# Performance work log

Hardware: AMD Instinct MI355X
Metric: run time of the kernel (lower is better)

The kernel has to match this reference:

```python
import jax, jax.numpy as jnp
import numpy as np

N_NODES = 50000
N_EDGES = 800000
N_GRAPHS = 128
HIDDEN = 64
HEADS = 2
OUT = 4
NEG_SLOPE = 0.2
ALPHA_FLAG = 0.05


def _gat_conv(x, src, dst, W, a_src, a_dst, b):
    # PyG GATConv, concat=False (mean over heads), self-loops already appended.
    N = x.shape[0]
    H, C = a_src.shape
    xh = (x @ W).reshape(N, H, C)                       # [N,H,C]
    s_src = (xh * a_src).sum(-1)                        # [N,H]
    s_dst = (xh * a_dst).sum(-1)                        # [N,H]
    e = s_src[src] + s_dst[dst]                         # [E,H]
    e = jnp.where(e > 0, e, NEG_SLOPE * e)              # LeakyReLU(0.2)
    emax = jax.ops.segment_max(e, dst, num_segments=N)  # per-dst softmax max
    emax = jnp.where(jnp.isfinite(emax), emax, 0.0)
    p = jnp.exp(e - emax[dst])
    denom = jax.ops.segment_sum(p, dst, num_segments=N)
    alpha = p / (denom[dst] + 1e-16)                    # [E,H]
    out = jax.ops.segment_sum(alpha[:, :, None] * xh[src], dst, num_segments=N)
    return out.mean(axis=1) + b                         # [N,HIDDEN]


def setup_inputs() -> dict:
    key = jax.random.key(0)
    ks = jax.random.split(key, 32)
    f = lambda k, shape, s=0.1: (jax.random.normal(k, shape) * s).astype(jnp.float32)
    inp = {}
    inp['x_all'] = jax.random.normal(ks[0], (N_NODES, 8), dtype=jnp.float32)
    inp['climber'] = jax.random.normal(ks[1], (N_GRAPHS, 4), dtype=jnp.float32)
    inp['edge_index'] = jax.random.randint(ks[2], (2, N_EDGES), 0, N_NODES)
    inp['batch'] = jnp.sort(jax.random.randint(ks[3], (N_NODES,), 0, N_GRAPHS))
    H = HIDDEN
    inp['W_in'] = f(ks[4], (6, H)); inp['b_in'] = jnp.zeros((H,), jnp.float32)
    inp['W_c'] = f(ks[5], (4, H)); inp['b_c'] = jnp.zeros((H,), jnp.float32)
    inp['W_f1'] = f(ks[6], (H, 2 * H)); inp['b_f1'] = jnp.zeros((2 * H,), jnp.float32)
    inp['W_f2'] = f(ks[7], (H, 2 * H)); inp['b_f2'] = jnp.zeros((2 * H,), jnp.float32)
    inp['W_g1'] = f(ks[8], (H, HEADS * H)); inp['a_src1'] = f(ks[9], (HEADS, H)); inp['a_dst1'] = f(ks[10], (HEADS, H)); inp['b_g1'] = jnp.zeros((H,), jnp.float32)
    inp['W_g2'] = f(ks[11], (H, HEADS * H)); inp['a_src2'] = f(ks[12], (HEADS, H)); inp['a_dst2'] = f(ks[13], (HEADS, H)); inp['b_g2'] = jnp.zeros((H,), jnp.float32)
    inp['W_cl1'] = f(ks[14], (H, H)); inp['b_cl1'] = jnp.zeros((H,), jnp.float32)
    inp['W_cl2'] = f(ks[15], (H, OUT)); inp['b_cl2'] = jnp.zeros((OUT,), jnp.float32)
    inp['W_fh1'] = f(ks[16], (2, 8), 0.001); inp['b_fh1'] = jnp.zeros((8,), jnp.float32)
    inp['W_fh2'] = f(ks[17], (8, OUT), 0.001); inp['b_fh2'] = jnp.zeros((OUT,), jnp.float32)
    return inp


def reference(x_all, climber, edge_index, batch, W_in, b_in, W_c, b_c,
              W_f1, b_f1, W_f2, b_f2,
              W_g1, a_src1, a_dst1, b_g1,
              W_g2, a_src2, a_dst2, b_g2,
              W_cl1, b_cl1, W_cl2, b_cl2,
              W_fh1, b_fh1, W_fh2, b_fh2):
    N = x_all.shape[0]
    flags = x_all[:, -2:]
    x = x_all[:, :-2]
    # climber embedding (eval mode -> dropout is identity)
    c = jax.nn.relu(climber @ W_c + b_c)                 # [G,H]
    x = x @ W_in + b_in                                  # [N,H]
    # FiLM 1
    gb = c @ W_f1 + b_f1
    gamma, beta = jnp.split(gb, 2, axis=-1)
    x = x * (1.0 + gamma[batch]) + beta[batch]
    # add self-loops (PyG GATConv default)
    loop = jnp.arange(N, dtype=edge_index.dtype)
    src = jnp.concatenate([edge_index[0], loop])
    dst = jnp.concatenate([edge_index[1], loop])
    x = jax.nn.relu(_gat_conv(x, src, dst, W_g1, a_src1, a_dst1, b_g1))
    # FiLM 2
    gb = c @ W_f2 + b_f2
    gamma, beta = jnp.split(gb, 2, axis=-1)
    x = x * (1.0 + gamma[batch]) + beta[batch]
    x = jax.nn.relu(_gat_conv(x, src, dst, W_g2, a_src2, a_dst2, b_g2))
    logits_main = jax.nn.relu(x @ W_cl1 + b_cl1) @ W_cl2 + b_cl2
    logits_flag = jax.nn.relu(flags @ W_fh1 + b_fh1) @ W_fh2 + b_fh2
    return logits_main + ALPHA_FLAG * logits_flag
```

## Files before the change

### kernel.cpp

```cpp
#include <hip/hip_runtime.h>
#include <hip/hip_fp16.h>

#define NEG_SLOPE 0.2f
#define ALPHA_FLAG 0.05f

static inline size_t align256(size_t x) { return (x + 255) & ~(size_t)255; }

__global__ void prep_kernel(const float* __restrict__ climber,
                            const float* __restrict__ W_c, const float* __restrict__ b_c,
                            const float* __restrict__ W_f1, const float* __restrict__ b_f1,
                            const float* __restrict__ W_f2, const float* __restrict__ b_f2,
                            float* __restrict__ gb1, float* __restrict__ gb2) {
    __shared__ float c_sh[64];
    int g = blockIdx.x, t = threadIdx.x;
    if (t < 64) {
        float acc = b_c[t];
#pragma unroll
        for (int k = 0; k < 4; ++k) acc = fmaf(climber[g * 4 + k], W_c[k * 64 + t], acc);
        c_sh[t] = fmaxf(acc, 0.f);
    }
    __syncthreads();
    float a1 = b_f1[t], a2 = b_f2[t];
#pragma unroll 8
    for (int h = 0; h < 64; ++h) {
        float cv = c_sh[h];
        a1 = fmaf(cv, W_f1[h * 128 + t], a1);
        a2 = fmaf(cv, W_f2[h * 128 + t], a2);
    }
    gb1[g * 128 + t] = a1;
    gb2[g * 128 + t] = a2;
}

__global__ void node_in_kernel(const float* __restrict__ x_all, const int* __restrict__ batch,
                               const float* __restrict__ W_in, const float* __restrict__ b_in,
                               const float* __restrict__ gb1, float* __restrict__ x, int N) {
    int idx = blockIdx.x * blockDim.x + threadIdx.x;
    if (idx >= N * 64) return;
    int n = idx >> 6, j = idx & 63;
    float acc = b_in[j];
#pragma unroll
    for (int k = 0; k < 6; ++k) acc = fmaf(x_all[n * 8 + k], W_in[k * 64 + j], acc);
    int g = batch[n];
    float gamma = gb1[g * 128 + j], beta = gb1[g * 128 + 64 + j];
    x[idx] = acc * (1.f + gamma) + beta;
}

__global__ void init_counts_kernel(int* __restrict__ counts, int N) {
    int i = blockIdx.x * blockDim.x + threadIdx.x;
    if (i < N) counts[i] = 1;
}

__global__ void hist_kernel(const int* __restrict__ dst, int E, int* __restrict__ counts) {
    int i = blockIdx.x * blockDim.x + threadIdx.x;
    if (i < E) atomicAdd(&counts[dst[i]], 1);
}

#define SCAN_CHUNK 1024
__global__ void scan_partial_kernel(const int* __restrict__ counts, int* __restrict__ block_sums, int N) {
    __shared__ int sh[256];
    int b = blockIdx.x, t = threadIdx.x;
    int idx0 = b * SCAN_CHUNK + t * 4;
    int s = 0;
    if (idx0 + 3 < N) {
        int4 v = *(const int4*)&counts[idx0];
        s = v.x + v.y + v.z + v.w;
    } else {
#pragma unroll
        for (int u = 0; u < 4; ++u) if (idx0 + u < N) s += counts[idx0 + u];
    }
    sh[t] = s;
    __syncthreads();
#pragma unroll
    for (int off = 128; off; off >>= 1) {
        if (t < off) sh[t] += sh[t + off];
        __syncthreads();
    }
    if (t == 0) block_sums[b] = sh[0];
}

__global__ void scan_blocksums_kernel(const int* __restrict__ block_sums, int* __restrict__ block_bases,
                                      int nb, int* __restrict__ row_ptr, int N) {
    __shared__ int sh[256];
    int t = threadIdx.x;
    int v = (t < nb) ? block_sums[t] : 0;
    sh[t] = v;
    __syncthreads();
#pragma unroll
    for (int off = 1; off < 256; off <<= 1) {
        int add = (t >= off) ? sh[t - off] : 0;
        __syncthreads();
        sh[t] += add;
        __syncthreads();
    }
    if (t < nb) block_bases[t] = sh[t] - v;
    if (t == nb - 1) row_ptr[N] = sh[t];
}

__global__ void scan_final_kernel(const int* __restrict__ counts, const int* __restrict__ block_bases,
                                  int* __restrict__ row_ptr, int* __restrict__ fill, int N) {
    __shared__ int sh[256];
    int b = blockIdx.x, t = threadIdx.x;
    int idx0 = b * SCAN_CHUNK + t * 4;
    int c[4];
    if (idx0 + 3 < N) {
        int4 v = *(const int4*)&counts[idx0];
        c[0] = v.x; c[1] = v.y; c[2] = v.z; c[3] = v.w;
    } else {
#pragma unroll
        for (int u = 0; u < 4; ++u) c[u] = (idx0 + u < N) ? counts[idx0 + u] : 0;
    }
    int s = c[0] + c[1] + c[2] + c[3];
    sh[t] = s;
    __syncthreads();
#pragma unroll
    for (int off = 1; off < 256; off <<= 1) {
        int add = (t >= off) ? sh[t - off] : 0;
        __syncthreads();
        sh[t] += add;
        __syncthreads();
    }
    int run = block_bases[b] + sh[t] - s;
#pragma unroll
    for (int u = 0; u < 4; ++u) {
        if (idx0 + u < N) {
            row_ptr[idx0 + u] = run;
            fill[idx0 + u] = run;
            run += c[u];
        }
    }
}

__global__ void scatter_kernel(const int* __restrict__ src, const int* __restrict__ dst,
                               int E, int N, int* __restrict__ fill, int* __restrict__ csr_src) {
    int i = blockIdx.x * blockDim.x + threadIdx.x;
    if (i >= E + N) return;
    int s, d;
    if (i < E) { s = src[i]; d = dst[i]; }
    else       { s = i - E; d = s; }
    int pos = atomicAdd(&fill[d], 1);
    csr_src[pos] = s;
}

#define XH_NB 32
__global__ __launch_bounds__(256, 4) void xh_kernel(
    const float* __restrict__ x, const float* __restrict__ W_g,
    const float* __restrict__ a_src, const float* __restrict__ a_dst,
    __half* __restrict__ xh, float* __restrict__ s_src, float* __restrict__ s_dst,
    int N) {
    __shared__ float x_sh[XH_NB * 64];
    int t = threadIdx.x;
    int base = blockIdx.x * XH_NB;
    {
        int nvalid = N - base; if (nvalid > XH_NB) nvalid = XH_NB;
        int nfloats = nvalid * 64;
#pragma unroll
        for (int rep = 0; rep < 2; ++rep) {
            int i = t * 4 + rep * 1024;
            float4 v = (i < nfloats) ? *(const float4*)&x[(size_t)base * 64 + i]
                                     : make_float4(0.f, 0.f, 0.f, 0.f);
            *(float4*)&x_sh[i] = v;
        }
    }
    __syncthreads();
    int c = t & 63;
    int g = t >> 6;
    float acc0[8], acc1[8];
#pragma unroll
    for (int i = 0; i < 8; ++i) { acc0[i] = 0.f; acc1[i] = 0.f; }
    const float* W0 = W_g + c;
    const float* W1 = W_g + 64 + c;
#pragma unroll 2
    for (int k = 0; k < 64; k += 4) {
        float w0[4], w1[4];
#pragma unroll
        for (int u = 0; u < 4; ++u) { w0[u] = W0[(k + u) * 128]; w1[u] = W1[(k + u) * 128]; }
#pragma unroll
        for (int i = 0; i < 8; ++i) {
            float4 xv = *(const float4*)&x_sh[(g * 8 + i) * 64 + k];
            acc0[i] = fmaf(xv.x, w0[0], acc0[i]);
            acc0[i] = fmaf(xv.y, w0[1], acc0[i]);
            acc0[i] = fmaf(xv.z, w0[2], acc0[i]);
            acc0[i] = fmaf(xv.w, w0[3], acc0[i]);
            acc1[i] = fmaf(xv.x, w1[0], acc1[i]);
            acc1[i] = fmaf(xv.y, w1[1], acc1[i]);
            acc1[i] = fmaf(xv.z, w1[2], acc1[i]);
            acc1[i] = fmaf(xv.w, w1[3], acc1[i]);
        }
    }
    float as0 = a_src[c], ad0 = a_dst[c];
    float as1 = a_src[64 + c], ad1 = a_dst[64 + c];
#pragma unroll
    for (int i = 0; i < 8; ++i) {
        int n = base + g * 8 + i;
        float ps0 = acc0[i] * as0, pd0 = acc0[i] * ad0;
        float ps1 = acc1[i] * as1, pd1 = acc1[i] * ad1;
#pragma unroll
        for (int off = 32; off; off >>= 1) {
            ps0 += __shfl_xor(ps0, off); pd0 += __shfl_xor(pd0, off);
            ps1 += __shfl_xor(ps1, off); pd1 += __shfl_xor(pd1, off);
        }
        if (n < N) {
            if (c == 0) {
                s_src[n * 2 + 0] = ps0; s_src[n * 2 + 1] = ps1;
                s_dst[n * 2 + 0] = pd0; s_dst[n * 2 + 1] = pd1;
            }
            __half2 hv = __floats2half2_rn(acc0[i], acc1[i]);
            *(__half2*)&xh[(size_t)n * 128 + c * 2] = hv;
        }
    }
}

__global__ __launch_bounds__(256) void agg_kernel(
    const __half* __restrict__ xh, const float* __restrict__ s_src,
    const float* __restrict__ s_dst, const int* __restrict__ row_ptr,
    const int* __restrict__ csr_src, const float* __restrict__ b_g,
    const int* __restrict__ batch, const float* __restrict__ gb_film,
    float* __restrict__ xout, int N, int mode,
    const float* __restrict__ x_all,
    const float* __restrict__ W_cl1, const float* __restrict__ b_cl1,
    const float* __restrict__ W_cl2, const float* __restrict__ b_cl2,
    const float* __restrict__ W_fh1, const float* __restrict__ b_fh1,
    const float* __restrict__ W_fh2, const float* __restrict__ b_fh2,
    float* __restrict__ out) {
    __shared__ float4 ps_sh[4][64];
    __shared__ float v_sh[4][64];
    int lane = threadIdx.x & 63;
    int w = threadIdx.x >> 6;
    int n = (blockIdx.x * blockDim.x + threadIdx.x) >> 6;
    if (n >= N) return;
    int beg = row_ptr[n], end = row_ptr[n + 1];
    float2 sd = *(const float2*)&s_dst[n * 2];
    const char* xhb = (const char*)xh;
    unsigned lane4 = (unsigned)lane * 4u;
    float acc0 = 0.f, acc1 = 0.f, dp0 = 0.f, dp1 = 0.f;
    for (int chunk = beg; chunk < end; chunk += 64) {
        int m = end - chunk; if (m > 64) m = 64;
        float p0 = 0.f, p1 = 0.f; unsigned sb = 0;
        if (lane < m) {
            int s = csr_src[chunk + lane];
            sb = (unsigned)s << 8;
            float2 ss = *(const float2*)&s_src[s * 2];
            float e0 = ss.x + sd.x;
            float e1 = ss.y + sd.y;
            e0 = (e0 > 0.f) ? e0 : NEG_SLOPE * e0;
            e1 = (e1 > 0.f) ? e1 : NEG_SLOPE * e1;
            p0 = __expf(e0); p1 = __expf(e1);
        }
        dp0 += p0; dp1 += p1;
        ps_sh[w][lane] = make_float4(p0, p1, __uint_as_float(sb), 0.f);
        int mr = (m + 7) & ~7;
        for (int j = 0; j < mr; j += 8) {
            unsigned voff[8];
#pragma unroll
            for (int u = 0; u < 8; ++u)
                voff[u] = __float_as_uint(ps_sh[w][j + u].z) + lane4;
            float2 xf[8];
#pragma unroll
            for (int u = 0; u < 8; ++u) {
                __half2 hv = *(const __half2*)(xhb + voff[u]);
                xf[u] = __half22float2(hv);
            }
#pragma unroll
            for (int u = 0; u < 8; ++u) {
                float2 pq = *(const float2*)&ps_sh[w][j + u];
                acc0 = fmaf(pq.x, xf[u].x, acc0);
                acc1 = fmaf(pq.y, xf[u].y, acc1);
            }
        }
    }
#pragma unroll
    for (int off = 32; off; off >>= 1) {
        dp0 += __shfl_xor(dp0, off);
        dp1 += __shfl_xor(dp1, off);
    }
    float v = 0.5f * (acc0 / (dp0 + 1e-16f) + acc1 / (dp1 + 1e-16f)) + b_g[lane];
    v = fmaxf(v, 0.f);
    if (mode == 0) {
        int g = batch[n];
        v = v * (1.f + gb_film[g * 128 + lane]) + gb_film[g * 128 + 64 + lane];
        xout[(size_t)n * 64 + lane] = v;
        return;
    }
    v_sh[w][lane] = v;
    float h = b_cl1[lane];
#pragma unroll 4
    for (int k = 0; k < 64; k += 4) {
        float4 vq = *(const float4*)&v_sh[w][k];
        h = fmaf(vq.x, W_cl1[(k + 0) * 64 + lane], h);
        h = fmaf(vq.y, W_cl1[(k + 1) * 64 + lane], h);
        h = fmaf(vq.z, W_cl1[(k + 2) * 64 + lane], h);
        h = fmaf(vq.w, W_cl1[(k + 3) * 64 + lane], h);
    }
    h = fmaxf(h, 0.f);
    float4 w2 = *(const float4*)&W_cl2[lane * 4];
    float o0 = h * w2.x, o1 = h * w2.y, o2 = h * w2.z, o3 = h * w2.w;
#pragma unroll
    for (int off = 32; off; off >>= 1) {
        o0 += __shfl_xor(o0, off); o1 += __shfl_xor(o1, off);
        o2 += __shfl_xor(o2, off); o3 += __shfl_xor(o3, off);
    }
    if (lane < 4) {
        float f0 = x_all[(size_t)n * 8 + 6], f1 = x_all[(size_t)n * 8 + 7];
        float lf = b_fh2[lane];
#pragma unroll
        for (int m = 0; m < 8; ++m) {
            float fm = fmaxf(fmaf(f0, W_fh1[m], fmaf(f1, W_fh1[8 + m], b_fh1[m])), 0.f);
            lf = fmaf(fm, W_fh2[m * 4 + lane], lf);
        }
        float om = (lane == 0) ? o0 : (lane == 1) ? o1 : (lane == 2) ? o2 : o3;
        out[(size_t)n * 4 + lane] = om + b_cl2[lane] + ALPHA_FLAG * lf;
    }
}

extern "C" void kernel_launch(void* const* d_in, const int* in_sizes, int n_in,
                              void* d_out, int out_size, void* d_ws, size_t ws_size,
                              hipStream_t stream) {
    const float* x_all   = (const float*)d_in[0];
    const float* climber = (const float*)d_in[1];
    const int*   eidx    = (const int*)d_in[2];
    const int*   batch   = (const int*)d_in[3];
    const float* W_in  = (const float*)d_in[4];
    const float* b_in  = (const float*)d_in[5];
    const float* W_c   = (const float*)d_in[6];
    const float* b_c   = (const float*)d_in[7];
    const float* W_f1  = (const float*)d_in[8];
    const float* b_f1  = (const float*)d_in[9];
    const float* W_f2  = (const float*)d_in[10];
    const float* b_f2  = (const float*)d_in[11];
    const float* W_g1  = (const float*)d_in[12];
    const float* a_s1  = (const float*)d_in[13];
    const float* a_d1  = (const float*)d_in[14];
    const float* b_g1  = (const float*)d_in[15];
    const float* W_g2  = (const float*)d_in[16];
    const float* a_s2  = (const float*)d_in[17];
    const float* a_d2  = (const float*)d_in[18];
    const float* b_g2  = (const float*)d_in[19];
    const float* W_cl1 = (const float*)d_in[20];
    const float* b_cl1 = (const float*)d_in[21];
    const float* W_cl2 = (const float*)d_in[22];
    const float* b_cl2 = (const float*)d_in[23];
    const float* W_fh1 = (const float*)d_in[24];
    const float* b_fh1 = (const float*)d_in[25];
    const float* W_fh2 = (const float*)d_in[26];
    const float* b_fh2 = (const float*)d_in[27];
    float* out = (float*)d_out;

    const int N = in_sizes[0] / 8;
    const int E = in_sizes[2] / 2;
    const int G = in_sizes[1] / 4;
    const int* src = eidx;
    const int* dst = eidx + E;
    const int NB_SCAN = (N + SCAN_CHUNK - 1) / SCAN_CHUNK;

    char* ws = (char*)d_ws;
    size_t off = 0;
    auto alloc = [&](size_t bytes) { char* p = ws + off; off += align256(bytes); return p; };
    float*  gb1     = (float*)alloc((size_t)G * 128 * 4);
    float*  gb2     = (float*)alloc((size_t)G * 128 * 4);
    float*  xbuf    = (float*)alloc((size_t)N * 64 * 4);
    __half* xh      = (__half*)alloc((size_t)N * 128 * 2);
    float*  s_src   = (float*)alloc((size_t)N * 2 * 4);
    float*  s_dst   = (float*)alloc((size_t)N * 2 * 4);
    int*    counts  = (int*)alloc((size_t)N * 4);
    int*    fill    = (int*)alloc((size_t)N * 4);
    int*    row_ptr = (int*)alloc((size_t)(N + 1) * 4);
    int*    csr_src = (int*)alloc((size_t)(E + N) * 4);
    int*    bsums   = (int*)alloc((size_t)256 * 4);
    int*    bbases  = (int*)alloc((size_t)256 * 4);
    (void)ws_size;

    prep_kernel<<<G, 128, 0, stream>>>(climber, W_c, b_c, W_f1, b_f1, W_f2, b_f2, gb1, gb2);
    node_in_kernel<<<(N * 64 + 255) / 256, 256, 0, stream>>>(x_all, batch, W_in, b_in, gb1, xbuf, N);
    init_counts_kernel<<<(N + 255) / 256, 256, 0, stream>>>(counts, N);
    hist_kernel<<<(E + 255) / 256, 256, 0, stream>>>(dst, E, counts);
    scan_partial_kernel<<<NB_SCAN, 256, 0, stream>>>(counts, bsums, N);
    scan_blocksums_kernel<<<1, 256, 0, stream>>>(bsums, bbases, NB_SCAN, row_ptr, N);
    scan_final_kernel<<<NB_SCAN, 256, 0, stream>>>(counts, bbases, row_ptr, fill, N);
    scatter_kernel<<<(E + N + 255) / 256, 256, 0, stream>>>(src, dst, E, N, fill, csr_src);
    xh_kernel<<<(N + XH_NB - 1) / XH_NB, 256, 0, stream>>>(xbuf, W_g1, a_s1, a_d1, xh, s_src, s_dst, N);
    agg_kernel<<<(N * 64 + 255) / 256, 256, 0, stream>>>(xh, s_src, s_dst, row_ptr, csr_src,
                                                         b_g1, batch, gb2, xbuf, N, 0,
                                                         nullptr, nullptr, nullptr, nullptr,
                                                         nullptr, nullptr, nullptr, nullptr,
                                                         nullptr, nullptr);
    xh_kernel<<<(N + XH_NB - 1) / XH_NB, 256, 0, stream>>>(xbuf, W_g2, a_s2, a_d2, xh, s_src, s_dst, N);
    agg_kernel<<<(N * 64 + 255) / 256, 256, 0, stream>>>(xh, s_src, s_dst, row_ptr, csr_src,
                                                         b_g2, batch, nullptr, nullptr, N, 1,
                                                         x_all, W_cl1, b_cl1, W_cl2, b_cl2,
                                                         W_fh1, b_fh1, W_fh2, b_fh2, out);
}
```

Before: 265.1 us.

## Fuse input projection into first xh kernel and vectorize edge gathers

Removes the standalone node input/FiLM kernel and computes the input projection and FiLM directly into shared memory inside the first xh_kernel, avoiding a global write and re-read of the 50000x64 activation buffer and one launch. The aggregation kernel now processes four edges per wave iteration: each 16-lane group loads 16 bytes (8 halves) per edge with uint4 loads, instead of every lane loading 4 bytes per edge. Partial sums are reduced across groups with shuffles and rearranged through shared memory. This trades fewer, wider gather transactions for extra shuffles, more accumulator registers and padding waste when degrees are not multiples of four.

```diff
diff --git a/kernel.cpp b/kernel.cpp
--- a/kernel.cpp
+++ b/kernel.cpp
@@ -29,20 +29,6 @@
     }
     gb1[g * 128 + t] = a1;
     gb2[g * 128 + t] = a2;
-}
-
-__global__ void node_in_kernel(const float* __restrict__ x_all, const int* __restrict__ batch,
-                               const float* __restrict__ W_in, const float* __restrict__ b_in,
-                               const float* __restrict__ gb1, float* __restrict__ x, int N) {
-    int idx = blockIdx.x * blockDim.x + threadIdx.x;
-    if (idx >= N * 64) return;
-    int n = idx >> 6, j = idx & 63;
-    float acc = b_in[j];
-#pragma unroll
-    for (int k = 0; k < 6; ++k) acc = fmaf(x_all[n * 8 + k], W_in[k * 64 + j], acc);
-    int g = batch[n];
-    float gamma = gb1[g * 128 + j], beta = gb1[g * 128 + 64 + j];
-    x[idx] = acc * (1.f + gamma) + beta;
 }
 
 __global__ void init_counts_kernel(int* __restrict__ counts, int N) {
@@ -146,11 +132,40 @@
     const float* __restrict__ x, const float* __restrict__ W_g,
     const float* __restrict__ a_src, const float* __restrict__ a_dst,
     __half* __restrict__ xh, float* __restrict__ s_src, float* __restrict__ s_dst,
-    int N) {
+    int N, int in_mode,
+    const float* __restrict__ x_all, const int* __restrict__ batch,
+    const float* __restrict__ W_in, const float* __restrict__ b_in,
+    const float* __restrict__ gb1) {
     __shared__ float x_sh[XH_NB * 64];
+    __shared__ float win_sh[6 * 64 + 64];
     int t = threadIdx.x;
     int base = blockIdx.x * XH_NB;
-    {
+    if (in_mode) {
+        for (int i = t; i < 448; i += 256)
+            win_sh[i] = (i < 384) ? W_in[i] : b_in[i - 384];
+        __syncthreads();
+        int nd = t >> 3;
+        int jb = (t & 7) * 8;
+        int n = base + nd;
+        if (n < N) {
+            float4 a = *(const float4*)&x_all[(size_t)n * 8];
+            float2 b = *(const float2*)&x_all[(size_t)n * 8 + 4];
+            float xa[6] = {a.x, a.y, a.z, a.w, b.x, b.y};
+            int g = batch[n];
+            const float* gbrow = &gb1[g * 128];
+#pragma unroll
+            for (int jj = 0; jj < 8; ++jj) {
+                int j = jb + jj;
+                float acc = win_sh[384 + j];
+#pragma unroll
+                for (int k = 0; k < 6; ++k) acc = fmaf(xa[k], win_sh[k * 64 + j], acc);
+                x_sh[nd * 64 + j] = acc * (1.f + gbrow[j]) + gbrow[64 + j];
+            }
+        } else {
+#pragma unroll
+            for (int jj = 0; jj < 8; ++jj) x_sh[nd * 64 + jb + jj] = 0.f;
+        }
+    } else {
         int nvalid = N - base; if (nvalid > XH_NB) nvalid = XH_NB;
         int nfloats = nvalid * 64;
 #pragma unroll
@@ -223,7 +238,7 @@
     const float* __restrict__ W_fh2, const float* __restrict__ b_fh2,
     float* __restrict__ out) {
     __shared__ float4 ps_sh[4][64];
-    __shared__ float v_sh[4][64];
+    __shared__ float vh_sh[4][128];
     int lane = threadIdx.x & 63;
     int w = threadIdx.x >> 6;
     int n = (blockIdx.x * blockDim.x + threadIdx.x) >> 6;
@@ -231,8 +246,10 @@
     int beg = row_ptr[n], end = row_ptr[n + 1];
     float2 sd = *(const float2*)&s_dst[n * 2];
     const char* xhb = (const char*)xh;
-    unsigned lane4 = (unsigned)lane * 4u;
-    float acc0 = 0.f, acc1 = 0.f, dp0 = 0.f, dp1 = 0.f;
+    int sub = lane >> 4;
+    unsigned q16 = (unsigned)(lane & 15) * 16u;
+    float acc[8] = {0.f, 0.f, 0.f, 0.f, 0.f, 0.f, 0.f, 0.f};
+    float dp0 = 0.f, dp1 = 0.f;
     for (int chunk = beg; chunk < end; chunk += 64) {
         int m = end - chunk; if (m > 64) m = 64;
         float p0 = 0.f, p1 = 0.f; unsigned sb = 0;
@@ -248,32 +265,41 @@
         }
         dp0 += p0; dp1 += p1;
         ps_sh[w][lane] = make_float4(p0, p1, __uint_as_float(sb), 0.f);
-        int mr = (m + 7) & ~7;
-        for (int j = 0; j < mr; j += 8) {
-            unsigned voff[8];
-#pragma unroll
-            for (int u = 0; u < 8; ++u)
-                voff[u] = __float_as_uint(ps_sh[w][j + u].z) + lane4;
-            float2 xf[8];
-#pragma unroll
-            for (int u = 0; u < 8; ++u) {
-                __half2 hv = *(const __half2*)(xhb + voff[u]);
-                xf[u] = __half22float2(hv);
-            }
-#pragma unroll
-            for (int u = 0; u < 8; ++u) {
-                float2 pq = *(const float2*)&ps_sh[w][j + u];
-                acc0 = fmaf(pq.x, xf[u].x, acc0);
-                acc1 = fmaf(pq.y, xf[u].y, acc1);
-            }
-        }
+        int mr = (m + 3) & ~3;
+        for (int j = 0; j < mr; j += 4) {
+            float4 ps = ps_sh[w][j + sub];
+            unsigned voff = __float_as_uint(ps.z) + q16;
+            uint4 hv = *(const uint4*)(xhb + voff);
+            float2 c0 = __half22float2(*(__half2*)&hv.x);
+            float2 c1 = __half22float2(*(__half2*)&hv.y);
+            float2 c2 = __half22float2(*(__half2*)&hv.z);
+            float2 c3 = __half22float2(*(__half2*)&hv.w);
+            acc[0] = fmaf(ps.x, c0.x, acc[0]); acc[1] = fmaf(ps.y, c0.y, acc[1]);
+            acc[2] = fmaf(ps.x, c1.x, acc[2]); acc[3] = fmaf(ps.y, c1.y, acc[3]);
+            acc[4] = fmaf(ps.x, c2.x, acc[4]); acc[5] = fmaf(ps.y, c2.y, acc[5]);
+            acc[6] = fmaf(ps.x, c3.x, acc[6]); acc[7] = fmaf(ps.y, c3.y, acc[7]);
+        }
+    }
+#pragma unroll
+    for (int u = 0; u < 8; ++u) {
+        acc[u] += __shfl_xor(acc[u], 16);
+        acc[u] += __shfl_xor(acc[u], 32);
     }
 #pragma unroll
     for (int off = 32; off; off >>= 1) {
         dp0 += __shfl_xor(dp0, off);
         dp1 += __shfl_xor(dp1, off);
     }
-    float v = 0.5f * (acc0 / (dp0 + 1e-16f) + acc1 / (dp1 + 1e-16f)) + b_g[lane];
+    if (lane < 16) {
+        int q4 = lane * 4;
+        vh_sh[w][q4 + 0] = acc[0]; vh_sh[w][q4 + 1] = acc[2];
+        vh_sh[w][q4 + 2] = acc[4]; vh_sh[w][q4 + 3] = acc[6];
+        vh_sh[w][64 + q4 + 0] = acc[1]; vh_sh[w][64 + q4 + 1] = acc[3];
+        vh_sh[w][64 + q4 + 2] = acc[5]; vh_sh[w][64 + q4 + 3] = acc[7];
+    }
+    float A0 = vh_sh[w][lane];
+    float A1 = vh_sh[w][64 + lane];
+    float v = 0.5f * (A0 / (dp0 + 1e-16f) + A1 / (dp1 + 1e-16f)) + b_g[lane];
     v = fmaxf(v, 0.f);
     if (mode == 0) {
         int g = batch[n];
@@ -281,11 +307,11 @@
         xout[(size_t)n * 64 + lane] = v;
         return;
     }
-    v_sh[w][lane] = v;
+    vh_sh[w][lane] = v;
     float h = b_cl1[lane];
 #pragma unroll 4
     for (int k = 0; k < 64; k += 4) {
-        float4 vq = *(const float4*)&v_sh[w][k];
+        float4 vq = *(const float4*)&vh_sh[w][k];
         h = fmaf(vq.x, W_cl1[(k + 0) * 64 + lane], h);
         h = fmaf(vq.y, W_cl1[(k + 1) * 64 + lane], h);
         h = fmaf(vq.z, W_cl1[(k + 2) * 64 + lane], h);
@@ -370,20 +396,23 @@
     (void)ws_size;
 
     prep_kernel<<<G, 128, 0, stream>>>(climber, W_c, b_c, W_f1, b_f1, W_f2, b_f2, gb1, gb2);
-    node_in_kernel<<<(N * 64 + 255) / 256, 256, 0, stream>>>(x_all, batch, W_in, b_in, gb1, xbuf, N);
     init_counts_kernel<<<(N + 255) / 256, 256, 0, stream>>>(counts, N);
     hist_kernel<<<(E + 255) / 256, 256, 0, stream>>>(dst, E, counts);
     scan_partial_kernel<<<NB_SCAN, 256, 0, stream>>>(counts, bsums, N);
     scan_blocksums_kernel<<<1, 256, 0, stream>>>(bsums, bbases, NB_SCAN, row_ptr, N);
     scan_final_kernel<<<NB_SCAN, 256, 0, stream>>>(counts, bbases, row_ptr, fill, N);
     scatter_kernel<<<(E + N + 255) / 256, 256, 0, stream>>>(src, dst, E, N, fill, csr_src);
-    xh_kernel<<<(N + XH_NB - 1) / XH_NB, 256, 0, stream>>>(xbuf, W_g1, a_s1, a_d1, xh, s_src, s_dst, N);
+    xh_kernel<<<(N + XH_NB - 1) / XH_NB, 256, 0, stream>>>(nullptr, W_g1, a_s1, a_d1, xh,
+                                                           s_src, s_dst, N, 1,
+                                                           x_all, batch, W_in, b_in, gb1);
     agg_kernel<<<(N * 64 + 255) / 256, 256, 0, stream>>>(xh, s_src, s_dst, row_ptr, csr_src,
                                                          b_g1, batch, gb2, xbuf, N, 0,
                                                          nullptr, nullptr, nullptr, nullptr,
                                                          nullptr, nullptr, nullptr, nullptr,
                                                          nullptr, nullptr);
-    xh_kernel<<<(N + XH_NB - 1) / XH_NB, 256, 0, stream>>>(xbuf, W_g2, a_s2, a_d2, xh, s_src, s_dst, N);
+    xh_kernel<<<(N + XH_NB - 1) / XH_NB, 256, 0, stream>>>(xbuf, W_g2, a_s2, a_d2, xh,
+                                                           s_src, s_dst, N, 0,
+                                                           nullptr, nullptr, nullptr, nullptr, nullptr);
     agg_kernel<<<(N * 64 + 255) / 256, 256, 0, stream>>>(xh, s_src, s_dst, row_ptr, csr_src,
                                                          b_g2, batch, nullptr, nullptr, N, 1,
                                                          x_all, W_cl1, b_cl1, W_cl2, b_cl2,
```

New measurement: 266.8 us. About the same (+0.6%).
